# Kernel optimization log

Hardware: AMD Instinct MI355X
Metric: run time of the kernel (lower is better)

Reference implementation:

```python
import jax, jax.numpy as jnp
import numpy as np

EMBED = 512
HEADS = 8


def setup_inputs() -> dict:
    key = jax.random.key(0)
    ks = jax.random.split(key, 9)
    s = 1.0 / np.sqrt(EMBED)
    inp = {
        "x": jax.random.normal(ks[0], (2, 4096, EMBED), dtype=jnp.float32),
        "Wv": jax.random.normal(ks[1], (EMBED, EMBED), dtype=jnp.float32) * s,
        "bv": jnp.zeros((EMBED,), dtype=jnp.float32),
        "Wk": jax.random.normal(ks[2], (EMBED, EMBED), dtype=jnp.float32) * s,
        "bk": jnp.zeros((EMBED,), dtype=jnp.float32),
        "Wq": jax.random.normal(ks[3], (EMBED, EMBED), dtype=jnp.float32) * s,
        "bq": jnp.zeros((EMBED,), dtype=jnp.float32),
        "Wo": jax.random.normal(ks[4], (EMBED, EMBED), dtype=jnp.float32) * s,
        "bo": jnp.zeros((EMBED,), dtype=jnp.float32),
    }
    return inp


def reference(x, Wv, bv, Wk, bk, Wq, bq, Wo, bo):
    B, S, E = x.shape
    H = HEADS
    D = E // H
    # linear projections (torch Linear: x @ W.T + b)
    v = (x @ Wv.T + bv).reshape(B, S, H, D)
    k = (x @ Wk.T + bk).reshape(B, S, H, D)
    q = (x @ Wq.T + bq).reshape(B, S, H, D)
    # scores [B,H,S,S]; NOTE: source scales by 1/sqrt(embed_size), not sqrt(d_head)
    energy = jnp.einsum('bqhd,bkhd->bhqk', q, k)
    attn = jax.nn.softmax(energy / jnp.sqrt(jnp.asarray(E, x.dtype)), axis=3)
    out = jnp.einsum('bhqk,bkhd->bqhd', attn, v).reshape(B, S, E)
    return out @ Wo.T + bo
```

## Files before the change

### kernel.cpp

```cpp
#include <hip/hip_runtime.h>


typedef __bf16 bf16x8 __attribute__((ext_vector_type(8)));
typedef float f32x4 __attribute__((ext_vector_type(4)));
typedef float f32x16 __attribute__((ext_vector_type(16)));
typedef unsigned int u32x4 __attribute__((ext_vector_type(4)));
typedef unsigned short u16x4 __attribute__((ext_vector_type(4)));

union U8 { bf16x8 b; u32x4 q; unsigned short s[8]; };

__device__ __forceinline__ unsigned short f2bf(float f) {
    union { float f; unsigned u; } x; x.f = f;
    unsigned r = x.u + 0x7FFFu + ((x.u >> 16) & 1u);
    return (unsigned short)(r >> 16);
}

__device__ __forceinline__ unsigned cvtpk(float lo, float hi) {
    unsigned d;
    asm("v_cvt_pk_bf16_f32 %0, %1, %2" : "=v"(d) : "v"(lo), "v"(hi));
    return d;
}

#if __has_builtin(__builtin_amdgcn_exp2f)
__device__ __forceinline__ float hexp2(float x) { return __builtin_amdgcn_exp2f(x); }
#else
__device__ __forceinline__ float hexp2(float x) { return exp2f(x); }
#endif

__device__ __forceinline__ void stage16(const void* g, void* lds) {
    __builtin_amdgcn_global_load_lds(
        (const __attribute__((address_space(1))) unsigned*)g,
        (__attribute__((address_space(3))) unsigned*)lds, 16, 0, 0);
}

__device__ __forceinline__ f32x4 mfma16(bf16x8 a, bf16x8 b, f32x4 c) {
    return __builtin_amdgcn_mfma_f32_16x16x32_bf16(a, b, c, 0, 0, 0);
}
__device__ __forceinline__ f32x16 mfma32(bf16x8 a, bf16x8 b, f32x16 c) {
    return __builtin_amdgcn_mfma_f32_32x32x16_bf16(a, b, c, 0, 0, 0);
}

__global__ __launch_bounds__(256) void cvt_kernel(
    const float* __restrict__ x, const float* __restrict__ wq, const float* __restrict__ wk,
    const float* __restrict__ wv, const float* __restrict__ wo,
    unsigned short* __restrict__ xb, unsigned short* __restrict__ wqkv,
    unsigned short* __restrict__ wob)
{
    const int NX = 8192 * 512, NW = 512 * 512;
    const int total = NX + 4 * NW;
    for (int i = blockIdx.x * 256 + threadIdx.x; i < total; i += gridDim.x * 256) {
        if (i < NX) {
            xb[i] = f2bf(x[i]);
        } else if (i < NX + 3 * NW) {
            int j = i - NX; int p = j / NW; int r = j - p * NW;
            const float* w = (p == 0) ? wq : (p == 1) ? wk : wv;
            wqkv[j] = f2bf(w[r]);
        } else {
            int j = i - NX - 3 * NW;
            wob[j] = f2bf(wo[j]);
        }
    }
}

__global__ __launch_bounds__(256) void gemm_bt(
    const unsigned short* __restrict__ A, const unsigned short* __restrict__ Bw, int mode,
    const float* __restrict__ bias0, const float* __restrict__ bias1, const float* __restrict__ bias2,
    unsigned short* __restrict__ qo, unsigned short* __restrict__ ko, unsigned short* __restrict__ vto,
    float* __restrict__ outf)
{
    __shared__ unsigned short Al[128 * 64];
    __shared__ unsigned short Bl[128 * 64];
    const int tid = threadIdx.x;
    const int l = tid & 63, w = tid >> 6;
    const int l15 = l & 15, g = l >> 4;
    const int m0 = blockIdx.y * 128, n0 = blockIdx.x * 128;
    const int mo = (w >> 1) * 64, no = (w & 1) * 64;
    f32x4 acc[4][4] = {};

    for (int k0 = 0; k0 < 512; k0 += 64) {
        __syncthreads();
        #pragma unroll
        for (int i = 0; i < 4; ++i) {
            int off = i * 4096 + w * 1024 + l * 16;
            int row = off >> 7;
            int c = (l & 7) ^ (row & 7);
            stage16(A + (m0 + row) * 512 + k0 + c * 8, (char*)Al + i * 4096 + w * 1024);
            stage16(Bw + (n0 + row) * 512 + k0 + c * 8, (char*)Bl + i * 4096 + w * 1024);
        }
        __syncthreads();
        #pragma unroll
        for (int ks = 0; ks < 2; ++ks) {
            U8 af[4];
            #pragma unroll
            for (int mt = 0; mt < 4; ++mt) {
                int row = mo + mt * 16 + l15;
                int c = (ks * 4 + g) ^ (row & 7);
                af[mt].q = *(const u32x4*)((const char*)Al + row * 128 + c * 16);
            }
            #pragma unroll
            for (int nt = 0; nt < 4; ++nt) {
                int row = no + nt * 16 + l15;
                int c = (ks * 4 + g) ^ (row & 7);
                U8 bf; bf.q = *(const u32x4*)((const char*)Bl + row * 128 + c * 16);
                #pragma unroll
                for (int mt = 0; mt < 4; ++mt)
                    acc[mt][nt] = mfma16(af[mt].b, bf.b, acc[mt][nt]);
            }
        }
    }

    if (mode == 0) {
        const float QSC = 0.06375871897178588f;
        #pragma unroll
        for (int nt = 0; nt < 4; ++nt) {
            int n = n0 + no + nt * 16 + l15;
            int proj = n >> 9, nn = n & 511;
            int h = nn >> 6, d = nn & 63;
            const float* bp = (proj == 0) ? bias0 : (proj == 1) ? bias1 : bias2;
            float bv_ = bp[nn];
            #pragma unroll
            for (int mt = 0; mt < 4; ++mt) {
                int m = m0 + mo + mt * 16 + g * 4;
                int bb = m >> 12, s = m & 4095;
                if (proj == 0) {
                    unsigned short* dst = qo + ((bb * 8 + h) * 4096 + s) * 64 + d;
                    #pragma unroll
                    for (int r = 0; r < 4; ++r)
                        dst[r * 64] = f2bf((acc[mt][nt][r] + bv_) * QSC);
                } else if (proj == 1) {
                    unsigned short* dst = ko + ((bb * 8 + h) * 4096 + s) * 64 + d;
                    #pragma unroll
                    for (int r = 0; r < 4; ++r)
                        dst[r * 64] = f2bf(acc[mt][nt][r] + bv_);
                } else {
                    u16x4 v4;
                    v4.x = f2bf(acc[mt][nt][0] + bv_);
                    v4.y = f2bf(acc[mt][nt][1] + bv_);
                    v4.z = f2bf(acc[mt][nt][2] + bv_);
                    v4.w = f2bf(acc[mt][nt][3] + bv_);
                    *(u16x4*)(vto + ((bb * 8 + h) * 64 + d) * 4096 + s) = v4;
                }
            }
        }
    } else {
        #pragma unroll
        for (int nt = 0; nt < 4; ++nt) {
            int n = n0 + no + nt * 16 + l15;
            float bv_ = bias0[n];
            #pragma unroll
            for (int mt = 0; mt < 4; ++mt) {
                int m = m0 + mo + mt * 16 + g * 4;
                float* dst = outf + (size_t)m * 512 + n;
                #pragma unroll
                for (int r = 0; r < 4; ++r)
                    dst[(size_t)r * 512] = acc[mt][nt][r] + bv_;
            }
        }
    }
}

__global__ __launch_bounds__(512, 4) void attn_kernel(
    const unsigned short* __restrict__ Qg, const unsigned short* __restrict__ Kg,
    const unsigned short* __restrict__ Vtg, unsigned short* __restrict__ Og)
{
    __shared__ __align__(16) char ldsb[65536];
    const int tid = threadIdx.x;
    const int l = tid & 63, w = tid >> 6;
    const int l31 = l & 31, hi = l >> 5;
    const int hb = w >> 2, w4 = w & 3;

    const int xcd = blockIdx.x & 7, idx = blockIdx.x >> 3;
    const int bh = xcd * 2 + (idx >> 5), qb = idx & 31;

    const unsigned short* qh = Qg + bh * 4096 * 64;
    const char* khb = (const char*)(Kg + (size_t)bh * 4096 * 64);
    const char* vhb = (const char*)(Vtg + (size_t)bh * 64 * 4096);
    const int qw = qb * 128 + w4 * 32;

    U8 Qf[4];
    #pragma unroll
    for (int ds_ = 0; ds_ < 4; ++ds_)
        Qf[ds_].q = *(const u32x4*)(qh + (qw + l31) * 64 + ds_ * 16 + hi * 8);

    int rd[4];
    #pragma unroll
    for (int j = 0; j < 4; ++j) {
        int sl = ((l31 & 1) << 3) + j * 2 + hi;
        int sp = sl ^ (l31 >> 1);
        rd[j] = hb * 16384 + (l31 >> 1) * 256 + sp * 16;
    }

    const char* ksrc0; const char* ksrc1; const char* vsrc0; const char* vsrc1;
    {
        int q0 = (w4 * 2 + 0) * 1024 + l * 16;
        int q1 = (w4 * 2 + 1) * 1024 + l * 16;
        int R0 = q0 >> 8, sl0 = ((q0 >> 4) & 15) ^ (R0 & 15);
        int R1 = q1 >> 8, sl1 = ((q1 >> 4) & 15) ^ (R1 & 15);
        int row0 = 2 * R0 + (sl0 >> 3), c0 = sl0 & 7;
        int row1 = 2 * R1 + (sl1 >> 3), c1 = sl1 & 7;
        ksrc0 = khb + (size_t)(hb * 2048 + row0) * 128 + c0 * 16;
        ksrc1 = khb + (size_t)(hb * 2048 + row1) * 128 + c1 * 16;
        vsrc0 = vhb + (size_t)row0 * 8192 + hb * 4096 + c0 * 16;
        vsrc1 = vhb + (size_t)row1 * 8192 + hb * 4096 + c1 * 16;
    }

    f32x16 oacc[2] = {};
    float lrun = 0.f;

    stage16(ksrc0, ldsb + hb * 16384 + (w4 * 2 + 0) * 1024);
    stage16(ksrc1, ldsb + hb * 16384 + (w4 * 2 + 1) * 1024);
    stage16(vsrc0, ldsb + hb * 16384 + 8192 + (w4 * 2 + 0) * 1024);
    stage16(vsrc1, ldsb + hb * 16384 + 8192 + (w4 * 2 + 1) * 1024);
    ksrc0 += 8192; ksrc1 += 8192; vsrc0 += 128; vsrc1 += 128;
    __syncthreads();

#define CHUNK(T_, PAR_) {                                                          \
    if ((T_) != 31) {                                                              \
        stage16(ksrc0, ldsb + (1 - (PAR_)) * 32768 + hb * 16384 + (w4 * 2 + 0) * 1024); \
        stage16(ksrc1, ldsb + (1 - (PAR_)) * 32768 + hb * 16384 + (w4 * 2 + 1) * 1024); \
        stage16(vsrc0, ldsb + (1 - (PAR_)) * 32768 + hb * 16384 + 8192 + (w4 * 2 + 0) * 1024); \
        stage16(vsrc1, ldsb + (1 - (PAR_)) * 32768 + hb * 16384 + 8192 + (w4 * 2 + 1) * 1024); \
    }                                                                              \
    ksrc0 += 8192; ksrc1 += 8192; vsrc0 += 128; vsrc1 += 128;                      \
    f32x16 et[2]; { f32x16 z = {}; et[0] = z; et[1] = z; }                         \
    __builtin_amdgcn_s_setprio(1);                                                 \
    _Pragma("unroll")                                                              \
    for (int ds_ = 0; ds_ < 4; ++ds_) {                                            \
        U8 kf0, kf1;                                                               \
        kf0.q = *(const u32x4*)(ldsb + (PAR_) * 32768 + rd[ds_]);                  \
        kf1.q = *(const u32x4*)(ldsb + (PAR_) * 32768 + 4096 + rd[ds_]);           \
        et[0] = mfma32(kf0.b, Qf[ds_].b, et[0]);                                   \
        et[1] = mfma32(kf1.b, Qf[ds_].b, et[1]);                                   \
    }                                                                              \
    __builtin_amdgcn_s_setprio(0);                                                 \
    float rs = 0.f;                                                                \
    _Pragma("unroll")                                                              \
    for (int ks = 0; ks < 4; ++ks) {                                               \
        const int mt_ = ks >> 1, r0_ = (ks & 1) * 8;                               \
        float p0 = hexp2(et[mt_][r0_ + 0]);                                        \
        float p1 = hexp2(et[mt_][r0_ + 1]);                                        \
        float p2 = hexp2(et[mt_][r0_ + 2]);                                        \
        float p3 = hexp2(et[mt_][r0_ + 3]);                                        \
        float p4 = hexp2(et[mt_][r0_ + 4]);                                        \
        float p5 = hexp2(et[mt_][r0_ + 5]);                                        \
        float p6 = hexp2(et[mt_][r0_ + 6]);                                        \
        float p7 = hexp2(et[mt_][r0_ + 7]);                                        \
        rs += ((p0 + p1) + (p2 + p3)) + ((p4 + p5) + (p6 + p7));                   \
        unsigned X0 = cvtpk(p0, p1), X1 = cvtpk(p2, p3);                           \
        unsigned Y0 = cvtpk(p4, p5), Y1 = cvtpk(p6, p7);                           \
        asm volatile("v_permlane32_swap_b32 %0, %1" : "+v"(X0), "+v"(Y0));         \
        asm volatile("v_permlane32_swap_b32 %0, %1" : "+v"(X1), "+v"(Y1));         \
        U8 pb_; pb_.q.x = X0; pb_.q.y = X1; pb_.q.z = Y0; pb_.q.w = Y1;            \
        U8 vf0, vf1;                                                               \
        vf0.q = *(const u32x4*)(ldsb + (PAR_) * 32768 + 8192 + rd[ks]);            \
        vf1.q = *(const u32x4*)(ldsb + (PAR_) * 32768 + 8192 + 4096 + rd[ks]);     \
        __builtin_amdgcn_s_setprio(1);                                             \
        oacc[0] = mfma32(vf0.b, pb_.b, oacc[0]);                                   \
        oacc[1] = mfma32(vf1.b, pb_.b, oacc[1]);                                   \
        __builtin_amdgcn_s_setprio(0);                                             \
    }                                                                              \
    lrun += rs;                \
    __syncthreads();                                                               \
}

    #pragma unroll 1
    for (int t2 = 0; t2 < 16; ++t2) {
        CHUNK(2 * t2, 0)
        CHUNK(2 * t2 + 1, 1)
    }
#undef CHUNK

    lrun += __shfl_xor(lrun, 32, 64);

    if (w >= 4) {
        char* ob = ldsb + (w4 * 64 + l) * 128;
        #pragma unroll
        for (int dt = 0; dt < 2; ++dt)
            #pragma unroll
            for (int j = 0; j < 4; ++j) {
                int c = (dt * 4 + j) ^ (l & 7);
                f32x4 v4;
                v4[0] = oacc[dt][j * 4 + 0]; v4[1] = oacc[dt][j * 4 + 1];
                v4[2] = oacc[dt][j * 4 + 2]; v4[3] = oacc[dt][j * 4 + 3];
                *(f32x4*)(ob + c * 16) = v4;
            }
        if (hi == 0)
            *(float*)(ldsb + 32768 + (w4 * 32 + l31) * 4) = lrun;
    }
    __syncthreads();
    if (w < 4) {
        float l2 = *(const float*)(ldsb + 32768 + (w4 * 32 + l31) * 4);
        float inv = 1.f / (lrun + l2);
        const int b = bh >> 3, h = bh & 7;
        const int s = qw + l31;
        unsigned short* dst = Og + ((size_t)(b * 4096 + s)) * 512 + h * 64;
        const char* ob = ldsb + (w4 * 64 + l) * 128;
        #pragma unroll
        for (int dt = 0; dt < 2; ++dt)
            #pragma unroll
            for (int j = 0; j < 4; ++j) {
                int c = (dt * 4 + j) ^ (l & 7);
                f32x4 o2 = *(const f32x4*)(ob + c * 16);
                int d0 = dt * 32 + j * 8 + hi * 4;
                u16x4 v4;
                v4.x = f2bf((oacc[dt][j * 4 + 0] + o2[0]) * inv);
                v4.y = f2bf((oacc[dt][j * 4 + 1] + o2[1]) * inv);
                v4.z = f2bf((oacc[dt][j * 4 + 2] + o2[2]) * inv);
                v4.w = f2bf((oacc[dt][j * 4 + 3] + o2[3]) * inv);
                *(u16x4*)(dst + d0) = v4;
            }
    }
}

extern "C" void kernel_launch(void* const* d_in, const int* in_sizes, int n_in,
                              void* d_out, int out_size, void* d_ws, size_t ws_size,
                              hipStream_t stream)
{
    const float* x  = (const float*)d_in[0];
    const float* Wv = (const float*)d_in[1];
    const float* bv = (const float*)d_in[2];
    const float* Wk = (const float*)d_in[3];
    const float* bk = (const float*)d_in[4];
    const float* Wq = (const float*)d_in[5];
    const float* bq = (const float*)d_in[6];
    const float* Wo = (const float*)d_in[7];
    const float* bo = (const float*)d_in[8];
    float* out = (float*)d_out;

    char* p = (char*)d_ws;
    unsigned short* xb   = (unsigned short*)p; p += (size_t)8192 * 512 * 2;
    unsigned short* wqkv = (unsigned short*)p; p += (size_t)1536 * 512 * 2;
    unsigned short* wob  = (unsigned short*)p; p += (size_t)512 * 512 * 2;
    unsigned short* qa   = (unsigned short*)p; p += (size_t)16 * 4096 * 64 * 2;
    unsigned short* ka   = (unsigned short*)p; p += (size_t)16 * 4096 * 64 * 2;
    unsigned short* vta  = (unsigned short*)p; p += (size_t)16 * 4096 * 64 * 2;
    unsigned short* ao   = xb;

    cvt_kernel<<<4096, 256, 0, stream>>>(x, Wq, Wk, Wv, Wo, xb, wqkv, wob);

    dim3 gq(12, 64);
    gemm_bt<<<gq, 256, 0, stream>>>(xb, wqkv, 0, bq, bk, bv, qa, ka, vta, nullptr);

    attn_kernel<<<512, 512, 0, stream>>>(qa, ka, vta, ao);

    dim3 go(4, 64);
    gemm_bt<<<go, 256, 0, stream>>>(ao, wob, 1, bo, nullptr, nullptr, nullptr, nullptr, nullptr, out);
}
```

Measured before the change: 125.2 us.

## Vectorize conversion, add smaller-tile output GEMM, compute softmax row sums via MFMA

```diff
diff --git a/kernel.cpp b/kernel.cpp
--- a/kernel.cpp
+++ b/kernel.cpp
@@ -46,27 +46,30 @@
     unsigned short* __restrict__ xb, unsigned short* __restrict__ wqkv,
     unsigned short* __restrict__ wob)
 {
-    const int NX = 8192 * 512, NW = 512 * 512;
+    const int NX = 8192 * 512 / 4, NW = 512 * 512 / 4;
     const int total = NX + 4 * NW;
     for (int i = blockIdx.x * 256 + threadIdx.x; i < total; i += gridDim.x * 256) {
+        float4 v; unsigned short* dst;
         if (i < NX) {
-            xb[i] = f2bf(x[i]);
+            v = ((const float4*)x)[i]; dst = xb + i * 4;
         } else if (i < NX + 3 * NW) {
             int j = i - NX; int p = j / NW; int r = j - p * NW;
             const float* w = (p == 0) ? wq : (p == 1) ? wk : wv;
-            wqkv[j] = f2bf(w[r]);
+            v = ((const float4*)w)[r]; dst = wqkv + j * 4;
         } else {
             int j = i - NX - 3 * NW;
-            wob[j] = f2bf(wo[j]);
-        }
+            v = ((const float4*)wo)[j]; dst = wob + j * 4;
+        }
+        u16x4 o;
+        o.x = f2bf(v.x); o.y = f2bf(v.y); o.z = f2bf(v.z); o.w = f2bf(v.w);
+        *(u16x4*)dst = o;
     }
 }
 
 __global__ __launch_bounds__(256) void gemm_bt(
-    const unsigned short* __restrict__ A, const unsigned short* __restrict__ Bw, int mode,
+    const unsigned short* __restrict__ A, const unsigned short* __restrict__ Bw,
     const float* __restrict__ bias0, const float* __restrict__ bias1, const float* __restrict__ bias2,
-    unsigned short* __restrict__ qo, unsigned short* __restrict__ ko, unsigned short* __restrict__ vto,
-    float* __restrict__ outf)
+    unsigned short* __restrict__ qo, unsigned short* __restrict__ ko, unsigned short* __restrict__ vto)
 {
     __shared__ unsigned short Al[128 * 64];
     __shared__ unsigned short Bl[128 * 64];
@@ -109,52 +112,103 @@
         }
     }
 
-    if (mode == 0) {
-        const float QSC = 0.06375871897178588f;
-        #pragma unroll
-        for (int nt = 0; nt < 4; ++nt) {
-            int n = n0 + no + nt * 16 + l15;
-            int proj = n >> 9, nn = n & 511;
-            int h = nn >> 6, d = nn & 63;
-            const float* bp = (proj == 0) ? bias0 : (proj == 1) ? bias1 : bias2;
-            float bv_ = bp[nn];
-            #pragma unroll
-            for (int mt = 0; mt < 4; ++mt) {
-                int m = m0 + mo + mt * 16 + g * 4;
-                int bb = m >> 12, s = m & 4095;
-                if (proj == 0) {
-                    unsigned short* dst = qo + ((bb * 8 + h) * 4096 + s) * 64 + d;
-                    #pragma unroll
-                    for (int r = 0; r < 4; ++r)
-                        dst[r * 64] = f2bf((acc[mt][nt][r] + bv_) * QSC);
-                } else if (proj == 1) {
-                    unsigned short* dst = ko + ((bb * 8 + h) * 4096 + s) * 64 + d;
-                    #pragma unroll
-                    for (int r = 0; r < 4; ++r)
-                        dst[r * 64] = f2bf(acc[mt][nt][r] + bv_);
-                } else {
-                    u16x4 v4;
-                    v4.x = f2bf(acc[mt][nt][0] + bv_);
-                    v4.y = f2bf(acc[mt][nt][1] + bv_);
-                    v4.z = f2bf(acc[mt][nt][2] + bv_);
-                    v4.w = f2bf(acc[mt][nt][3] + bv_);
-                    *(u16x4*)(vto + ((bb * 8 + h) * 64 + d) * 4096 + s) = v4;
-                }
-            }
-        }
-    } else {
-        #pragma unroll
-        for (int nt = 0; nt < 4; ++nt) {
-            int n = n0 + no + nt * 16 + l15;
-            float bv_ = bias0[n];
-            #pragma unroll
-            for (int mt = 0; mt < 4; ++mt) {
-                int m = m0 + mo + mt * 16 + g * 4;
-                float* dst = outf + (size_t)m * 512 + n;
+    const float QSC = 0.06375871897178588f;
+    #pragma unroll
+    for (int nt = 0; nt < 4; ++nt) {
+        int n = n0 + no + nt * 16 + l15;
+        int proj = n >> 9, nn = n & 511;
+        int h = nn >> 6, d = nn & 63;
+        const float* bp = (proj == 0) ? bias0 : (proj == 1) ? bias1 : bias2;
+        float bv_ = bp[nn];
+        #pragma unroll
+        for (int mt = 0; mt < 4; ++mt) {
+            int m = m0 + mo + mt * 16 + g * 4;
+            int bb = m >> 12, s = m & 4095;
+            if (proj == 0) {
+                unsigned short* dst = qo + ((bb * 8 + h) * 4096 + s) * 64 + d;
                 #pragma unroll
                 for (int r = 0; r < 4; ++r)
-                    dst[(size_t)r * 512] = acc[mt][nt][r] + bv_;
-            }
+                    dst[r * 64] = f2bf((acc[mt][nt][r] + bv_) * QSC);
+            } else if (proj == 1) {
+                unsigned short* dst = ko + ((bb * 8 + h) * 4096 + s) * 64 + d;
+                #pragma unroll
+                for (int r = 0; r < 4; ++r)
+                    dst[r * 64] = f2bf(acc[mt][nt][r] + bv_);
+            } else {
+                u16x4 v4;
+                v4.x = f2bf(acc[mt][nt][0] + bv_);
+                v4.y = f2bf(acc[mt][nt][1] + bv_);
+                v4.z = f2bf(acc[mt][nt][2] + bv_);
+                v4.w = f2bf(acc[mt][nt][3] + bv_);
+                *(u16x4*)(vto + ((bb * 8 + h) * 64 + d) * 4096 + s) = v4;
+            }
+        }
+    }
+}
+
+__global__ __launch_bounds__(256) void gemm_o(
+    const unsigned short* __restrict__ A, const unsigned short* __restrict__ Bw,
+    const float* __restrict__ bias, float* __restrict__ outf)
+{
+    __shared__ unsigned short Al[64 * 64];
+    __shared__ unsigned short Bl[128 * 64];
+    const int tid = threadIdx.x;
+    const int l = tid & 63, w = tid >> 6;
+    const int l15 = l & 15, g = l >> 4;
+    const int m0 = blockIdx.y * 64, n0 = blockIdx.x * 128;
+    const int mo = (w >> 1) * 32, no = (w & 1) * 64;
+    f32x4 acc[2][4] = {};
+
+    for (int k0 = 0; k0 < 512; k0 += 64) {
+        __syncthreads();
+        #pragma unroll
+        for (int i = 0; i < 2; ++i) {
+            int jj = w * 2 + i;
+            int off = jj * 1024 + l * 16;
+            int row = off >> 7;
+            int c = (l & 7) ^ (row & 7);
+            stage16(A + (m0 + row) * 512 + k0 + c * 8, (char*)Al + jj * 1024);
+        }
+        #pragma unroll
+        for (int i = 0; i < 4; ++i) {
+            int jj = w * 4 + i;
+            int off = jj * 1024 + l * 16;
+            int row = off >> 7;
+            int c = (l & 7) ^ (row & 7);
+            stage16(Bw + (n0 + row) * 512 + k0 + c * 8, (char*)Bl + jj * 1024);
+        }
+        __syncthreads();
+        #pragma unroll
+        for (int ks = 0; ks < 2; ++ks) {
+            U8 af[2];
+            #pragma unroll
+            for (int mt = 0; mt < 2; ++mt) {
+                int row = mo + mt * 16 + l15;
+                int c = (ks * 4 + g) ^ (row & 7);
+                af[mt].q = *(const u32x4*)((const char*)Al + row * 128 + c * 16);
+            }
+            #pragma unroll
+            for (int nt = 0; nt < 4; ++nt) {
+                int row = no + nt * 16 + l15;
+                int c = (ks * 4 + g) ^ (row & 7);
+                U8 bf; bf.q = *(const u32x4*)((const char*)Bl + row * 128 + c * 16);
+                #pragma unroll
+                for (int mt = 0; mt < 2; ++mt)
+                    acc[mt][nt] = mfma16(af[mt].b, bf.b, acc[mt][nt]);
+            }
+        }
+    }
+    #pragma unroll
+    for (int nt = 0; nt < 4; ++nt) {
+        int n = n0 + no + nt * 16 + l15;
+        float bv_ = bias[n];
+        #pragma unroll
+        for (int mt = 0; mt < 2; ++mt) {
+            int m = m0 + mo + mt * 16 + g * 4;
+            float* dst = outf + (size_t)m * 512 + n;
+            #pragma unroll
+            for (int r = 0; r < 4; ++r)
+                dst[(size_t)r * 512] = acc[mt][nt][r] + bv_;
         }
     }
 }
@@ -181,6 +235,10 @@
     #pragma unroll
     for (int ds_ = 0; ds_ < 4; ++ds_)
         Qf[ds_].q = *(const u32x4*)(qh + (qw + l31) * 64 + ds_ * 16 + hi * 8);
+
+    U8 onev;
+    onev.q.x = 0x3F803F80u; onev.q.y = 0x3F803F80u;
+    onev.q.z = 0x3F803F80u; onev.q.w = 0x3F803F80u;
 
     int rd[4];
     #pragma unroll
@@ -205,7 +263,7 @@
     }
 
     f32x16 oacc[2] = {};
-    float lrun = 0.f;
+    f32x16 lacc = {};
 
     stage16(ksrc0, ldsb + hb * 16384 + (w4 * 2 + 0) * 1024);
     stage16(ksrc1, ldsb + hb * 16384 + (w4 * 2 + 1) * 1024);
@@ -233,7 +291,6 @@
         et[1] = mfma32(kf1.b, Qf[ds_].b, et[1]);                                   \
     }                                                                              \
     __builtin_amdgcn_s_setprio(0);                                                 \
-    float rs = 0.f;                                                                \
     _Pragma("unroll")                                                              \
     for (int ks = 0; ks < 4; ++ks) {                                               \
         const int mt_ = ks >> 1, r0_ = (ks & 1) * 8;                               \
@@ -245,7 +302,6 @@
         float p5 = hexp2(et[mt_][r0_ + 5]);                                        \
         float p6 = hexp2(et[mt_][r0_ + 6]);                                        \
         float p7 = hexp2(et[mt_][r0_ + 7]);                                        \
-        rs += ((p0 + p1) + (p2 + p3)) + ((p4 + p5) + (p6 + p7));                   \
         unsigned X0 = cvtpk(p0, p1), X1 = cvtpk(p2, p3);                           \
         unsigned Y0 = cvtpk(p4, p5), Y1 = cvtpk(p6, p7);                           \
         asm volatile("v_permlane32_swap_b32 %0, %1" : "+v"(X0), "+v"(Y0));         \
@@ -257,9 +313,9 @@
         __builtin_amdgcn_s_setprio(1);                                             \
         oacc[0] = mfma32(vf0.b, pb_.b, oacc[0]);                                   \
         oacc[1] = mfma32(vf1.b, pb_.b, oacc[1]);                                   \
+        lacc    = mfma32(onev.b, pb_.b, lacc);                                     \
         __builtin_amdgcn_s_setprio(0);                                             \
     }                                                                              \
-    lrun += rs;                \
     __syncthreads();                                                               \
 }
 
@@ -270,7 +326,7 @@
     }
 #undef CHUNK
 
-    lrun += __shfl_xor(lrun, 32, 64);
+    float lrun = lacc[0];
 
     if (w >= 4) {
         char* ob = ldsb + (w4 * 64 + l) * 128;
@@ -336,13 +392,13 @@
     unsigned short* vta  = (unsigned short*)p; p += (size_t)16 * 4096 * 64 * 2;
     unsigned short* ao   = xb;
 
-    cvt_kernel<<<4096, 256, 0, stream>>>(x, Wq, Wk, Wv, Wo, xb, wqkv, wob);
+    cvt_kernel<<<2048, 256, 0, stream>>>(x, Wq, Wk, Wv, Wo, xb, wqkv, wob);
 
     dim3 gq(12, 64);
-    gemm_bt<<<gq, 256, 0, stream>>>(xb, wqkv, 0, bq, bk, bv, qa, ka, vta, nullptr);
+    gemm_bt<<<gq, 256, 0, stream>>>(xb, wqkv, bq, bk, bv, qa, ka, vta);
 
     attn_kernel<<<512, 512, 0, stream>>>(qa, ka, vta, ao);
 
-    dim3 go(4, 64);
-    gemm_bt<<<go, 256, 0, stream>>>(ao, wob, 1, bo, nullptr, nullptr, nullptr, nullptr, nullptr, out);
-}
+    dim3 go(4, 128);
+    gemm_o<<<go, 256, 0, stream>>>(ao, wob, bo, out);
+}
```

New measurement: 123.7 us. About the same (-1.2%).
